# Kernel optimization log

Hardware: AMD Instinct MI355X
Metric: run time of the kernel (lower is better)

The kernel has to match this reference:

```python
import jax, jax.numpy as jnp
import numpy as np

DIM = 512
HEADS = 8
B, H, W = 8, 32, 32
SMOOTH = 1e-4
BN_EPS = 1e-5


def _conv(x, w, pad):
    return jax.lax.conv_general_dilated(
        x, w, window_strides=(1, 1), padding=[(pad, pad), (pad, pad)],
        dimension_numbers=('NCHW', 'OIHW', 'NCHW'))


def setup_inputs() -> dict:
    key = jax.random.key(0)
    k1, k2, k3 = jax.random.split(key, 3)
    x = jax.random.normal(k1, (B, DIM, H, W), dtype=jnp.float32)
    # conv weights with fan-in style scaling for stable magnitudes
    W_qkv = jax.random.normal(k2, (3 * DIM, DIM, 3, 3), dtype=jnp.float32) * (1.0 / np.sqrt(DIM * 9))
    W_out = jax.random.normal(k3, (DIM, DIM, 1, 1), dtype=jnp.float32) * (1.0 / np.sqrt(DIM))
    gamma = jnp.ones((DIM,), dtype=jnp.float32)
    beta = jnp.zeros((DIM,), dtype=jnp.float32)
    return {"x": x, "W_qkv": W_qkv, "W_out": W_out, "gamma": gamma, "beta": beta}


def reference(x, W_qkv, W_out, gamma, beta):
    b, c, h, w = x.shape
    g = HEADS
    d = c // g
    n = h * w
    qkv = _conv(x, W_qkv, pad=1)                      # [b, 3c, h, w]
    q, k, v = jnp.split(qkv, 3, axis=1)
    # 'b (g d) h w -> b g (h w) d'
    to_seq = lambda t: t.reshape(b, g, d, n).transpose(0, 1, 3, 2)
    q, k, v = to_seq(q), to_seq(k), to_seq(v)         # [b, g, n, d]
    attn = jnp.einsum('bgid,bgjd->bgij', q, k)        # [b, g, n, n]
    qn = jnp.sqrt(jnp.sum(q * q, axis=-1) + SMOOTH)   # [b, g, n]
    kn = jnp.sqrt(jnp.sum(k * k, axis=-1) + SMOOTH)   # [b, g, n]
    attn = attn / (qn[:, :, :, None] * kn[:, :, None, :] + SMOOTH)
    out = jnp.einsum('bgij,bgjd->bgid', attn, v)      # [b, g, n, d]
    # 'b g (h w) d -> b (g d) h w'
    out = out.transpose(0, 1, 3, 2).reshape(b, c, h, w)
    out = _conv(out, W_out, pad=0)
    # BatchNorm2d (training mode: batch statistics, biased variance)
    mean = jnp.mean(out, axis=(0, 2, 3))
    var = jnp.var(out, axis=(0, 2, 3))
    out = (out - mean[None, :, None, None]) * jax.lax.rsqrt(var + BN_EPS)[None, :, None, None]
    out = out * gamma[None, :, None, None] + beta[None, :, None, None]
    return jax.nn.relu(out)
```

## Files before the change

kernel.cpp:

```cpp
#include <hip/hip_runtime.h>
#include <math.h>


#define SMOOTH 1e-4f
#define BN_EPS 1e-5f

typedef __attribute__((ext_vector_type(8))) short bf16x8;
typedef __attribute__((ext_vector_type(8))) unsigned short u16x8;
typedef __attribute__((ext_vector_type(4))) float f32x4;
typedef __attribute__((ext_vector_type(16))) float f32x16;
typedef __attribute__((ext_vector_type(4))) unsigned int u32x4;
typedef __attribute__((ext_vector_type(4))) unsigned short u16x4;

__device__ inline unsigned short bf16rne(float f) {
  unsigned int u = __float_as_uint(f);
  u += 0x7fff + ((u >> 16) & 1);
  return (unsigned short)(u >> 16);
}
__device__ inline float b2f(unsigned short u) {
  return __uint_as_float((unsigned int)u << 16);
}

typedef __attribute__((address_space(1))) void gvoid;
typedef __attribute__((address_space(3))) void lvoid;
__device__ __forceinline__ void async16(const void* g, void* l) {
  __builtin_amdgcn_global_load_lds((gvoid*)g, (lvoid*)l, 16, 0, 0);
}

__global__ void prep_kernel(const float* __restrict__ wq,
                            unsigned short* __restrict__ wqr2,
                            const float* __restrict__ x,
                            unsigned short* __restrict__ xrp2,
                            const float* __restrict__ wo,
                            unsigned short* __restrict__ wor,
                            float* __restrict__ sums,
                            float* __restrict__ sumsq) {
  __shared__ float Sh[64 * 132];
  const int tid = threadIdx.x;
  const int bid = blockIdx.x;
  if (bid < 3072) {
    const size_t pair0 = (size_t)bid * 256;
    for (int off = tid; off < 576; off += 256)
      *(float4*)(Sh + off * 4) = *(const float4*)(wq + pair0 * 9 + off * 4);
    __syncthreads();
    const int co = (int)(pair0 >> 9);
    const int ciBase = (int)(pair0 & 511);
    const int cotile = co >> 6, co_l = co & 63;
    for (int idx = tid; idx < 288; idx += 256) {
      int t = idx >> 5;
      int oct = idx & 31;
      int ci = ciBase + oct * 8;
      int ci0c = ci >> 5, c4 = oct & 3;
      u16x8 pk;
#pragma unroll
      for (int e = 0; e < 8; ++e) pk[e] = bf16rne(Sh[(oct * 8 + e) * 9 + t]);
      size_t o = (size_t)(ci0c * 24 + cotile) * 18432 +
                 (size_t)((c4 * 9 + t) * 64 + co_l) * 8;
      *(u16x8*)(wqr2 + o) = pk;
    }
  } else if (bid < 3584) {
    const int bx = bid - 3072;
    const int p0 = (bx & 7) * 128;
    const int ci0 = ((bx >> 3) & 7) * 64;
    const int b = bx >> 6;
    for (int k = 0; k < 8; ++k) {
      int idx = tid + k * 256;
      int c4 = idx & 31, row = idx >> 5;
      *(float4*)(Sh + row * 132 + c4 * 4) =
          *(const float4*)(x + ((size_t)(b * 512 + ci0 + row)) * 1024 + p0 + c4 * 4);
    }
    __syncthreads();
    const int pl = tid >> 1, half = tid & 1;
    const int p = p0 + pl;
    const int h = p >> 5, w = p & 31;
#pragma unroll
    for (int v = 0; v < 8; ++v) {
      u16x4 pk;
#pragma unroll
      for (int e = 0; e < 4; ++e)
        pk[e] = bf16rne(Sh[(half * 32 + v * 4 + e) * 132 + pl]);
      int cc = ci0 + half * 32 + v * 4;
      int ci0c = cc >> 5, c4 = (cc >> 3) & 3, e0 = cc & 7;
      size_t gran =
          (size_t)((ci0c * 4 + c4) * 8 + b) * 1156 + (h + 1) * 34 + (w + 1);
      *(u16x4*)(xrp2 + gran * 8 + e0) = pk;
    }
  } else {
    const int rb = bid - 3584;
    int idx = rb * 256 + tid;
    wor[idx] = bf16rne(wo[idx]);
    if (rb < 2) {
      sums[idx] = 0.f;
      sumsq[idx] = 0.f;
    }
  }
}

__global__ __launch_bounds__(256) void conv3x3_mfma(
    const unsigned short* __restrict__ wqr2,
    const unsigned short* __restrict__ xrp2,
    unsigned short* __restrict__ qt, unsigned short* __restrict__ kt,
    unsigned short* __restrict__ vt, float* __restrict__ rqn,
    float* __restrict__ rkn) {
  __shared__ __align__(16) unsigned short Wl[2304 * 8];
  __shared__ __align__(16) unsigned short Xl[1360 * 8];

  const int tid = threadIdx.x;
  const int lane = tid & 63;
  const int wave = tid >> 6;
  const int l31 = lane & 31;
  const int hi = lane >> 5;
  const int wn = wave * 64;
  const int h0 = blockIdx.x * 8;
  const int co0 = blockIdx.y * 64;
  const int b = blockIdx.z;

  f32x16 acc[2][2];
  for (int ma = 0; ma < 2; ++ma)
    for (int nbt = 0; nbt < 2; ++nbt)
#pragma unroll
      for (int e = 0; e < 16; ++e) acc[ma][nbt][e] = 0.f;

  for (int ci0 = 0; ci0 < 512; ci0 += 32) {
    const int ci0c = ci0 >> 5;
    __syncthreads();
    const unsigned short* wsrc = wqr2 + (size_t)(ci0c * 24 + (co0 >> 6)) * 18432;
#pragma unroll
    for (int j = 0; j < 9; ++j) {
      int c = wave * 9 + j;
      async16(wsrc + (size_t)c * 512 + lane * 8, Wl + (size_t)c * 512);
    }
    const unsigned short* xsrc =
        xrp2 + ((size_t)((ci0c * 4 + wave) * 8 + b) * 1156 + h0 * 34) * 8;
#pragma unroll
    for (int j = 0; j < 5; ++j)
      async16(xsrc + (size_t)j * 512 + lane * 8,
              Xl + (size_t)(wave * 340 + j * 64) * 8);
    async16(xsrc + (size_t)276 * 8 + lane * 8, Xl + (size_t)(wave * 340 + 276) * 8);
    __syncthreads();

#pragma unroll
    for (int t = 0; t < 9; ++t) {
      const int ky = t / 3, kx = t - ky * 3;
      bf16x8 af[2][2], bfr[2][2];
#pragma unroll
      for (int s = 0; s < 2; ++s) {
        const int pl = (s * 2 + hi);
#pragma unroll
        for (int ma = 0; ma < 2; ++ma)
          af[ma][s] = *(const bf16x8*)(
              Wl + (size_t)(pl * 576 + t * 64 + ma * 32 + l31) * 8);
#pragma unroll
        for (int nbt = 0; nbt < 2; ++nbt) {
          int n = wn + nbt * 32 + l31;
          int hh = (n >> 5) + ky;
          int wi = (n & 31) + kx;
          bfr[nbt][s] = *(const bf16x8*)(Xl + (size_t)(pl * 340 + hh * 34 + wi) * 8);
        }
      }
#pragma unroll
      for (int s = 0; s < 2; ++s)
#pragma unroll
        for (int ma = 0; ma < 2; ++ma)
#pragma unroll
          for (int nbt = 0; nbt < 2; ++nbt)
            acc[ma][nbt] = __builtin_amdgcn_mfma_f32_32x32x16_bf16(
                af[ma][s], bfr[nbt][s], acc[ma][nbt], 0, 0, 0);
    }
  }

  const int sec = co0 >> 9;
  const int g = (co0 & 511) >> 6;
  const int bg = b * 8 + g;
  if (sec < 2) {
    unsigned short* dst = (sec == 0) ? qt : kt;
#pragma unroll
    for (int ma = 0; ma < 2; ++ma)
#pragma unroll
      for (int nbt = 0; nbt < 2; ++nbt) {
        int n = wn + nbt * 32 + l31;
        int p = (h0 + (n >> 5)) * 32 + (n & 31);
#pragma unroll
        for (int g4 = 0; g4 < 4; ++g4) {
          u16x4 pk;
#pragma unroll
          for (int r2 = 0; r2 < 4; ++r2) pk[r2] = bf16rne(acc[ma][nbt][g4 * 4 + r2]);
          int d = ma * 32 + g4 * 8 + hi * 4;
          *(u16x4*)(dst + ((size_t)bg * 1024 + p) * 64 + d) = pk;
        }
      }
    float sn[2];
#pragma unroll
    for (int nbt = 0; nbt < 2; ++nbt) {
      float s = 0.f;
#pragma unroll
      for (int ma = 0; ma < 2; ++ma)
#pragma unroll
        for (int e = 0; e < 16; ++e)
          s = fmaf(acc[ma][nbt][e], acc[ma][nbt][e], s);
      s += __shfl_down(s, 32);
      sn[nbt] = s;
    }
    if (lane < 32) {
      float* ndst = (sec == 0) ? rqn : rkn;
#pragma unroll
      for (int nbt = 0; nbt < 2; ++nbt) {
        int n = wn + nbt * 32 + lane;
        int p = (h0 + (n >> 5)) * 32 + (n & 31);
        ndst[bg * 1024 + p] = rsqrtf(sn[nbt] + SMOOTH);
      }
    }
  } else {
#pragma unroll
    for (int ma = 0; ma < 2; ++ma)
#pragma unroll
      for (int nbt = 0; nbt < 2; ++nbt) {
        int n = wn + nbt * 32 + l31;
        int p = (h0 + (n >> 5)) * 32 + (n & 31);
#pragma unroll
        for (int reg = 0; reg < 16; ++reg) {
          int d = ma * 32 + (reg & 3) + 8 * (reg >> 2) + 4 * hi;
          vt[((size_t)bg * 64 + d) * 1024 + p] = bf16rne(acc[ma][nbt][reg]);
        }
      }
  }
}

__global__ __launch_bounds__(256) void attn_mfma(
    const unsigned short* __restrict__ qt, const unsigned short* __restrict__ kt,
    const unsigned short* __restrict__ vt, const float* __restrict__ rqn,
    const float* __restrict__ rkn, unsigned short* __restrict__ aob) {
  __shared__ __align__(16) unsigned short Kl[64 * 72];
  __shared__ __align__(16) unsigned short Vl[64 * 72];
  __shared__ __align__(16) unsigned short Sl[64 * 72];

  const int tid = threadIdx.x;
  const int lane = tid & 63, wave = tid >> 6;
  const int l15 = lane & 15, quad = lane >> 4;
  const int bg = blockIdx.x;
  const int i0 = blockIdx.y * 64;
  const int iw = i0 + wave * 16;
  const int b = bg >> 3, g = bg & 7;

  bf16x8 qf[2];
#pragma unroll
  for (int ks = 0; ks < 2; ++ks)
    qf[ks] = *(const bf16x8*)(
        qt + ((size_t)bg * 1024 + iw + l15) * 64 + ks * 32 + quad * 8);

  float rq[4];
#pragma unroll
  for (int r = 0; r < 4; ++r) rq[r] = rqn[bg * 1024 + iw + quad * 4 + r];

  f32x4 oacc[4];
  for (int nf = 0; nf < 4; ++nf) oacc[nf] = (f32x4){0.f, 0.f, 0.f, 0.f};

  unsigned short* Sw = Sl + wave * 16 * 72;

  for (int jt = 0; jt < 16; ++jt) {
    const int j0 = jt * 64;
    __syncthreads();
    for (int idx = tid; idx < 512; idx += 256) {
      int c8 = idx & 7, row = idx >> 3;
      *(u32x4*)(Kl + row * 72 + c8 * 8) =
          *(const u32x4*)(kt + ((size_t)bg * 1024 + j0 + row) * 64 + c8 * 8);
      *(u32x4*)(Vl + row * 72 + c8 * 8) =
          *(const u32x4*)(vt + ((size_t)bg * 64 + row) * 1024 + j0 + c8 * 8);
    }
    __syncthreads();

    f32x4 sacc[4];
    for (int nb = 0; nb < 4; ++nb) sacc[nb] = (f32x4){0.f, 0.f, 0.f, 0.f};
#pragma unroll
    for (int ks = 0; ks < 2; ++ks) {
#pragma unroll
      for (int nb = 0; nb < 4; ++nb) {
        bf16x8 kf = *(const bf16x8*)(Kl + (l15 + 16 * nb) * 72 + ks * 32 + quad * 8);
        sacc[nb] = __builtin_amdgcn_mfma_f32_16x16x32_bf16(
            qf[ks], kf, sacc[nb], 0, 0, 0);
      }
    }

#pragma unroll
    for (int nb = 0; nb < 4; ++nb) {
      float rk = rkn[bg * 1024 + j0 + l15 + 16 * nb];
#pragma unroll
      for (int r = 0; r < 4; ++r) {
        float s = sacc[nb][r] * (rq[r] * rk);
        Sw[(quad * 4 + r) * 72 + l15 + 16 * nb] = bf16rne(s);
      }
    }
#pragma unroll
    for (int ks2 = 0; ks2 < 2; ++ks2) {
      bf16x8 sa = *(const bf16x8*)(Sw + l15 * 72 + ks2 * 32 + quad * 8);
#pragma unroll
      for (int nf = 0; nf < 4; ++nf) {
        bf16x8 vb = *(const bf16x8*)(Vl + (l15 + 16 * nf) * 72 + ks2 * 32 + quad * 8);
        oacc[nf] = __builtin_amdgcn_mfma_f32_16x16x32_bf16(sa, vb, oacc[nf], 0, 0, 0);
      }
    }
  }

#pragma unroll
  for (int nf = 0; nf < 4; ++nf)
#pragma unroll
    for (int r = 0; r < 4; ++r) {
      int i = iw + quad * 4 + r;
      int d = l15 + 16 * nf;
      aob[((size_t)(b * 1024) + i) * 512 + g * 64 + d] = bf16rne(oacc[nf][r]);
    }
}

__global__ __launch_bounds__(256) void conv1x1_mfma(
    const unsigned short* __restrict__ wor, const unsigned short* __restrict__ aob,
    unsigned short* __restrict__ yb, float* __restrict__ sums,
    float* __restrict__ sumsq) {
  __shared__ __align__(16) unsigned short Wl[64 * 40];
  __shared__ __align__(16) unsigned short Bl[64 * 40];

  const int tid = threadIdx.x;
  const int lane = tid & 63, wave = tid >> 6;
  const int l15 = lane & 15, quad = lane >> 4;
  const int wco = (wave & 1) * 32;
  const int wp = (wave >> 1) * 32;
  const int p0 = blockIdx.x * 64;
  const int co0 = blockIdx.y * 64;
  const int b = blockIdx.z;

  f32x4 acc[2][2];
  for (int ma = 0; ma < 2; ++ma)
    for (int nb = 0; nb < 2; ++nb) acc[ma][nb] = (f32x4){0.f, 0.f, 0.f, 0.f};

  for (int ci0 = 0; ci0 < 512; ci0 += 32) {
    __syncthreads();
    {
      int c4 = tid & 3, co = tid >> 2;
      *(u32x4*)(Wl + co * 40 + c4 * 8) =
          *(const u32x4*)(wor + (size_t)(co0 + co) * 512 + ci0 + c4 * 8);
      *(u32x4*)(Bl + co * 40 + c4 * 8) =
          *(const u32x4*)(aob + ((size_t)(b * 1024) + p0 + co) * 512 + ci0 + c4 * 8);
    }
    __syncthreads();

    bf16x8 af[2], bf[2];
#pragma unroll
    for (int ma = 0; ma < 2; ++ma)
      af[ma] = *(const bf16x8*)(Wl + (wco + ma * 16 + l15) * 40 + quad * 8);
#pragma unroll
    for (int nb = 0; nb < 2; ++nb)
      bf[nb] = *(const bf16x8*)(Bl + (wp + nb * 16 + l15) * 40 + quad * 8);
#pragma unroll
    for (int ma = 0; ma < 2; ++ma)
#pragma unroll
      for (int nb = 0; nb < 2; ++nb)
        acc[ma][nb] = __builtin_amdgcn_mfma_f32_16x16x32_bf16(
            af[ma], bf[nb], acc[ma][nb], 0, 0, 0);
  }

#pragma unroll
  for (int ma = 0; ma < 2; ++ma)
#pragma unroll
    for (int r = 0; r < 4; ++r) {
      int co = co0 + wco + ma * 16 + quad * 4 + r;
      float s1 = 0.f, s2 = 0.f;
#pragma unroll
      for (int nb = 0; nb < 2; ++nb) {
        float v = acc[ma][nb][r];
        yb[((size_t)(b * 512) + co) * 1024 + p0 + wp + nb * 16 + l15] = bf16rne(v);
        s1 += v;
        s2 = fmaf(v, v, s2);
      }
      for (int off = 8; off >= 1; off >>= 1) {
        s1 += __shfl_down(s1, off, 16);
        s2 += __shfl_down(s2, off, 16);
      }
      if (l15 == 0) {
        atomicAdd(&sums[co], s1);
        atomicAdd(&sumsq[co], s2);
      }
    }
}

__global__ void bn_kernel(const unsigned short* __restrict__ yb,
                          const float* __restrict__ sums,
                          const float* __restrict__ sumsq,
                          const float* __restrict__ gamma,
                          const float* __restrict__ beta,
                          float* __restrict__ out) {
  int idx = blockIdx.x * 256 + threadIdx.x;
  int c = (idx >> 8) & 511;
  u16x4 vb = *(const u16x4*)(yb + (size_t)idx * 4);
  float mean = sums[c] * (1.f / 8192.f);
  float var = sumsq[c] * (1.f / 8192.f) - mean * mean;
  float sc = gamma[c] * rsqrtf(var + BN_EPS);
  float sh = beta[c] - mean * sc;
  float4 r;
  r.x = fmaxf(0.f, fmaf(b2f(vb[0]), sc, sh));
  r.y = fmaxf(0.f, fmaf(b2f(vb[1]), sc, sh));
  r.z = fmaxf(0.f, fmaf(b2f(vb[2]), sc, sh));
  r.w = fmaxf(0.f, fmaf(b2f(vb[3]), sc, sh));
  ((float4*)out)[idx] = r;
}

extern "C" void kernel_launch(void* const* d_in, const int* in_sizes, int n_in,
                              void* d_out, int out_size, void* d_ws,
                              size_t ws_size, hipStream_t stream) {
  const float* x = (const float*)d_in[0];
  const float* wq = (const float*)d_in[1];
  const float* wo = (const float*)d_in[2];
  const float* gamma = (const float*)d_in[3];
  const float* beta = (const float*)d_in[4];
  float* out = (float*)d_out;

  unsigned short* qt = (unsigned short*)d_ws;
  unsigned short* kt = qt + (size_t)4194304;
  unsigned short* vt = kt + (size_t)4194304;
  unsigned short* aob = vt + (size_t)4194304;
  unsigned short* wqr2 = aob + (size_t)4194304;
  unsigned short* wor = wqr2 + (size_t)7077888;
  unsigned short* xrp2 = wor + (size_t)262144;
  float* rqn = (float*)(xrp2 + (size_t)4736000);
  float* rkn = rqn + 65536;
  unsigned short* yb = (unsigned short*)(rkn + 65536);
  float* sums = (float*)(yb + (size_t)4194304);
  float* sumsq = sums + 512;

  hipMemsetAsync(xrp2, 0, (size_t)4736000 * 2, stream);
  prep_kernel<<<dim3(4608), 256, 0, stream>>>(wq, wqr2, x, xrp2, wo, wor, sums,
                                              sumsq);
  conv3x3_mfma<<<dim3(4, 24, 8), 256, 0, stream>>>(wqr2, xrp2, qt, kt, vt, rqn,
                                                   rkn);
  attn_mfma<<<dim3(64, 16), 256, 0, stream>>>(qt, kt, vt, rqn, rkn, aob);
  conv1x1_mfma<<<dim3(16, 8, 8), 256, 0, stream>>>(wor, aob, yb, sums, sumsq);
  bn_kernel<<<dim3(4096), 256, 0, stream>>>(yb, sums, sumsq, gamma, beta, out);
}
```

Measured before the change: 294.2 us.

## Split conv3x3 into single-wave blocks over 2 rows and half-chunk K steps

The 3x3 conv kernel changes from 256-thread blocks covering 8 output rows to 64-thread single-wave blocks covering 2 rows. Each K iteration now loads half of a 32-channel chunk (16 channels), so there are 32 iterations instead of 16. The aim is to raise block count and occupancy and shrink shared memory per block so more blocks fit per CU. The cost is that each block reloads the full 64-output-channel weight slab, so weight traffic per output row goes up fourfold, and there are more barriers per MFMA.

```diff
diff --git a/kernel.cpp b/kernel.cpp
--- a/kernel.cpp
+++ b/kernel.cpp
@@ -96,22 +96,19 @@
   }
 }
 
-__global__ __launch_bounds__(256) void conv3x3_mfma(
+__global__ __launch_bounds__(64) void conv3x3_mfma(
     const unsigned short* __restrict__ wqr2,
     const unsigned short* __restrict__ xrp2,
     unsigned short* __restrict__ qt, unsigned short* __restrict__ kt,
     unsigned short* __restrict__ vt, float* __restrict__ rqn,
     float* __restrict__ rkn) {
-  __shared__ __align__(16) unsigned short Wl[2304 * 8];
-  __shared__ __align__(16) unsigned short Xl[1360 * 8];
-
-  const int tid = threadIdx.x;
-  const int lane = tid & 63;
-  const int wave = tid >> 6;
+  __shared__ __align__(16) unsigned short Wl[1152 * 8];
+  __shared__ __align__(16) unsigned short Xl[272 * 8];
+
+  const int lane = threadIdx.x;
   const int l31 = lane & 31;
   const int hi = lane >> 5;
-  const int wn = wave * 64;
-  const int h0 = blockIdx.x * 8;
+  const int h0 = blockIdx.x * 2;
   const int co0 = blockIdx.y * 64;
   const int b = blockIdx.z;
 
@@ -121,51 +118,47 @@
 #pragma unroll
       for (int e = 0; e < 16; ++e) acc[ma][nbt][e] = 0.f;
 
-  for (int ci0 = 0; ci0 < 512; ci0 += 32) {
-    const int ci0c = ci0 >> 5;
-    __syncthreads();
-    const unsigned short* wsrc = wqr2 + (size_t)(ci0c * 24 + (co0 >> 6)) * 18432;
-#pragma unroll
-    for (int j = 0; j < 9; ++j) {
-      int c = wave * 9 + j;
+  for (int kc = 0; kc < 32; ++kc) {
+    const int ci0c = kc >> 1;
+    const int half = kc & 1;
+    __syncthreads();
+    const unsigned short* wsrc =
+        wqr2 + (size_t)(ci0c * 24 + (co0 >> 6)) * 18432 + (size_t)half * 9216;
+#pragma unroll
+    for (int c = 0; c < 18; ++c)
       async16(wsrc + (size_t)c * 512 + lane * 8, Wl + (size_t)c * 512);
-    }
-    const unsigned short* xsrc =
-        xrp2 + ((size_t)((ci0c * 4 + wave) * 8 + b) * 1156 + h0 * 34) * 8;
-#pragma unroll
-    for (int j = 0; j < 5; ++j)
-      async16(xsrc + (size_t)j * 512 + lane * 8,
-              Xl + (size_t)(wave * 340 + j * 64) * 8);
-    async16(xsrc + (size_t)276 * 8 + lane * 8, Xl + (size_t)(wave * 340 + 276) * 8);
+#pragma unroll
+    for (int q = 0; q < 2; ++q) {
+      const unsigned short* xsrc =
+          xrp2 +
+          ((size_t)((ci0c * 4 + half * 2 + q) * 8 + b) * 1156 + h0 * 34) * 8;
+      async16(xsrc + (size_t)0 * 512 + lane * 8, Xl + (size_t)(q * 136) * 8);
+      async16(xsrc + (size_t)1 * 512 + lane * 8, Xl + (size_t)(q * 136 + 64) * 8);
+      async16(xsrc + (size_t)72 * 8 + lane * 8, Xl + (size_t)(q * 136 + 72) * 8);
+    }
     __syncthreads();
 
 #pragma unroll
     for (int t = 0; t < 9; ++t) {
       const int ky = t / 3, kx = t - ky * 3;
-      bf16x8 af[2][2], bfr[2][2];
-#pragma unroll
-      for (int s = 0; s < 2; ++s) {
-        const int pl = (s * 2 + hi);
-#pragma unroll
-        for (int ma = 0; ma < 2; ++ma)
-          af[ma][s] = *(const bf16x8*)(
-              Wl + (size_t)(pl * 576 + t * 64 + ma * 32 + l31) * 8);
-#pragma unroll
-        for (int nbt = 0; nbt < 2; ++nbt) {
-          int n = wn + nbt * 32 + l31;
-          int hh = (n >> 5) + ky;
-          int wi = (n & 31) + kx;
-          bfr[nbt][s] = *(const bf16x8*)(Xl + (size_t)(pl * 340 + hh * 34 + wi) * 8);
-        }
-      }
-#pragma unroll
-      for (int s = 0; s < 2; ++s)
-#pragma unroll
-        for (int ma = 0; ma < 2; ++ma)
-#pragma unroll
-          for (int nbt = 0; nbt < 2; ++nbt)
-            acc[ma][nbt] = __builtin_amdgcn_mfma_f32_32x32x16_bf16(
-                af[ma][s], bfr[nbt][s], acc[ma][nbt], 0, 0, 0);
+      bf16x8 af[2], bfr[2];
+#pragma unroll
+      for (int ma = 0; ma < 2; ++ma)
+        af[ma] = *(const bf16x8*)(
+            Wl + (size_t)((hi * 9 + t) * 64 + ma * 32 + l31) * 8);
+#pragma unroll
+      for (int nbt = 0; nbt < 2; ++nbt) {
+        int n = nbt * 32 + l31;
+        int hh = (n >> 5) + ky;
+        int wi = (n & 31) + kx;
+        bfr[nbt] = *(const bf16x8*)(Xl + (size_t)(hi * 136 + hh * 34 + wi) * 8);
+      }
+#pragma unroll
+      for (int ma = 0; ma < 2; ++ma)
+#pragma unroll
+        for (int nbt = 0; nbt < 2; ++nbt)
+          acc[ma][nbt] = __builtin_amdgcn_mfma_f32_32x32x16_bf16(
+              af[ma], bfr[nbt], acc[ma][nbt], 0, 0, 0);
     }
   }
 
@@ -178,13 +171,14 @@
     for (int ma = 0; ma < 2; ++ma)
 #pragma unroll
       for (int nbt = 0; nbt < 2; ++nbt) {
-        int n = wn + nbt * 32 + l31;
+        int n = nbt * 32 + l31;
         int p = (h0 + (n >> 5)) * 32 + (n & 31);
 #pragma unroll
         for (int g4 = 0; g4 < 4; ++g4) {
           u16x4 pk;
 #pragma unroll
-          for (int r2 = 0; r2 < 4; ++r2) pk[r2] = bf16rne(acc[ma][nbt][g4 * 4 + r2]);
+          for (int r2 = 0; r2 < 4; ++r2)
+            pk[r2] = bf16rne(acc[ma][nbt][g4 * 4 + r2]);
           int d = ma * 32 + g4 * 8 + hi * 4;
           *(u16x4*)(dst + ((size_t)bg * 1024 + p) * 64 + d) = pk;
         }
@@ -205,7 +199,7 @@
       float* ndst = (sec == 0) ? rqn : rkn;
 #pragma unroll
       for (int nbt = 0; nbt < 2; ++nbt) {
-        int n = wn + nbt * 32 + lane;
+        int n = nbt * 32 + lane;
         int p = (h0 + (n >> 5)) * 32 + (n & 31);
         ndst[bg * 1024 + p] = rsqrtf(sn[nbt] + SMOOTH);
       }
@@ -215,7 +209,7 @@
     for (int ma = 0; ma < 2; ++ma)
 #pragma unroll
       for (int nbt = 0; nbt < 2; ++nbt) {
-        int n = wn + nbt * 32 + l31;
+        int n = nbt * 32 + l31;
         int p = (h0 + (n >> 5)) * 32 + (n & 31);
 #pragma unroll
         for (int reg = 0; reg < 16; ++reg) {
@@ -428,7 +422,7 @@
   hipMemsetAsync(xrp2, 0, (size_t)4736000 * 2, stream);
   prep_kernel<<<dim3(4608), 256, 0, stream>>>(wq, wqr2, x, xrp2, wo, wor, sums,
                                               sumsq);
-  conv3x3_mfma<<<dim3(4, 24, 8), 256, 0, stream>>>(wqr2, xrp2, qt, kt, vt, rqn,
+  conv3x3_mfma<<<dim3(16, 24, 8), 64, 0, stream>>>(wqr2, xrp2, qt, kt, vt, rqn,
                                                    rkn);
   attn_mfma<<<dim3(64, 16), 256, 0, stream>>>(qt, kt, vt, rqn, rkn, aob);
   conv1x1_mfma<<<dim3(16, 8, 8), 256, 0, stream>>>(wor, aob, yb, sums, sumsq);
```

New measurement: 326.3 us. 1.11x slower.
